# Kernel tuning notes

Hardware: AMD Instinct MI355X
Metric: run time of the kernel (lower is better)

The kernel has to match this reference:

```python
import jax, jax.numpy as jnp
import numpy as np
from jax import lax

BATCH, FS, DIM = 32, 7, 512
E, TOPK, KD = 4, 2, 4            # experts, top-k, scan directions
N_STATE, DT_RANK = 16, 32
CAP_FACTOR, EPS, AUX_W = 1.25, 1e-6, 0.01


def _layernorm(x, g, b, eps=1e-5):
    mu = x.mean(-1, keepdims=True)
    var = ((x - mu) ** 2).mean(-1, keepdims=True)
    return (x - mu) * lax.rsqrt(var + eps) * g + b


def setup_inputs() -> dict:
    key = jax.random.key(0)
    ks = jax.random.split(key, 10)
    s = 0.02
    d = DIM
    return {
        "x": jax.random.normal(ks[0], (BATCH, FS, FS, d), jnp.float32),
        "w_gate": jax.random.normal(ks[1], (d, E)) * s,
        "b_gate": jnp.zeros((E,), jnp.float32),
        "in_proj_w": jax.random.normal(ks[2], (E, d, 2 * d)) * s,
        "in_proj_b": jnp.zeros((E, 2 * d), jnp.float32),
        "conv_w": jax.random.normal(ks[3], (E, d, 3, 3)) * s,
        "conv_b": jnp.zeros((E, d), jnp.float32),
        "x_proj_w": jax.random.normal(ks[4], (E, KD, DT_RANK + 2 * N_STATE, d)) * s,
        "dt_proj_w": jax.random.normal(ks[5], (E, KD, d, DT_RANK)) * s,
        "dt_proj_b": jax.random.normal(ks[6], (E, KD, d)) * 0.1,
        "A_log": jnp.log(jax.random.uniform(ks[7], (E, KD, d, N_STATE), minval=1.0, maxval=16.0)),
        "Ds": jnp.ones((E, KD, d), jnp.float32),
        "out_norm_g": jnp.ones((E, d), jnp.float32),
        "out_norm_b": jnp.zeros((E, d), jnp.float32),
        "norm_g": jnp.ones((E, d), jnp.float32),
        "norm_b": jnp.zeros((E, d), jnp.float32),
    }


def _ss2d_expert(x, in_w, in_b, cw, cb, xpw, dtw, dtb, A_log, Ds, og, ob, ng, nb):
    # x: [B,H,W,d]; one SS2D expert (VMamba-style, use_out_proj=False, out_norm=True)
    B, H, W, d = x.shape
    L = H * W
    xz = x @ in_w + in_b                      # [B,H,W,2d]
    xin, z = jnp.split(xz, 2, axis=-1)
    xc = jnp.transpose(xin, (0, 3, 1, 2))     # [B,d,H,W]
    xc = lax.conv_general_dilated(xc, cw[:, None, :, :], (1, 1), 'SAME',
                                  feature_group_count=d,
                                  dimension_numbers=('NCHW', 'OIHW', 'NCHW'))
    xc = jax.nn.silu(xc + cb[None, :, None, None])
    xh = xc.reshape(B, d, L)                              # row-major (h)
    xv = jnp.transpose(xc, (0, 1, 3, 2)).reshape(B, d, L)  # col-major (v)
    xs = jnp.stack([xh, xh[..., ::-1], xv, xv[..., ::-1]], axis=1)  # [B,K,d,L]

    x_dbl = jnp.einsum('bkdl,kcd->bkcl', xs, xpw)
    dt, Bm, Cm = jnp.split(x_dbl, [DT_RANK, DT_RANK + N_STATE], axis=2)
    dt = jnp.einsum('bkrl,kdr->bkdl', dt, dtw) + dtb[None, :, :, None]
    dt = jax.nn.softplus(dt)                  # [B,K,d,L]
    A = -jnp.exp(A_log)                       # [K,d,N]

    def step(h, inp):
        dt_t, B_t, C_t, x_t = inp             # [B,K,d],[B,K,N],[B,K,N],[B,K,d]
        h = h * jnp.exp(dt_t[..., None] * A) + (dt_t * x_t)[..., None] * B_t[:, :, None, :]
        y = jnp.einsum('bkdn,bkn->bkd', h, C_t)
        return h, y

    h0 = jnp.zeros((B, KD, d, N_STATE), x.dtype)
    seq = (jnp.moveaxis(dt, 3, 0), jnp.moveaxis(Bm, 3, 0),
           jnp.moveaxis(Cm, 3, 0), jnp.moveaxis(xs, 3, 0))
    _, ys = lax.scan(step, h0, seq)           # [L,B,K,d]
    ys = jnp.moveaxis(ys, 0, 3) + Ds[None, :, :, None] * xs  # [B,K,d,L]

    y = ys[:, 0] + ys[:, 1, :, ::-1]
    yv = ys[:, 2] + ys[:, 3, :, ::-1]
    y = y + jnp.transpose(yv.reshape(B, d, W, H), (0, 1, 3, 2)).reshape(B, d, L)
    y = jnp.transpose(y.reshape(B, d, H, W), (0, 2, 3, 1))   # [B,H,W,d]
    y = _layernorm(y, og, ob) * jax.nn.silu(z)
    pooled = y.mean(axis=(1, 2))              # adaptive avg pool -> [B,d]
    return _layernorm(pooled, ng, nb)


def reference(x, w_gate, b_gate, in_proj_w, in_proj_b, conv_w, conv_b, x_proj_w,
              dt_proj_w, dt_proj_b, A_log, Ds, out_norm_g, out_norm_b, norm_g, norm_b):
    B = x.shape[0]
    # gate on globally pooled features
    x_flat = x.mean(axis=(1, 2))                              # [B,dim]
    raw = jax.nn.softmax(x_flat @ w_gate + b_gate, axis=-1)   # [B,E]
    capacity = int(CAP_FACTOR * B)
    _, idx = lax.top_k(raw, TOPK)
    mask = jax.nn.one_hot(idx, E, dtype=raw.dtype).sum(axis=1)  # [B,E]
    masked = raw * mask
    denom = masked.sum(0, keepdims=True) + EPS
    gate_scores = masked / denom * capacity
    importance = raw.mean(0)
    load = mask.mean(0)
    aux_loss = AUX_W * jnp.mean((load - importance) ** 2)

    topv, topi = lax.top_k(gate_scores, TOPK)                 # [B,k]
    # dense dispatch: run every expert on the full batch (E small), then gather
    all_out = jax.vmap(_ss2d_expert, in_axes=(None,) + (0,) * 13)(
        x, in_proj_w, in_proj_b, conv_w, conv_b, x_proj_w, dt_proj_w, dt_proj_b,
        A_log, Ds, out_norm_g, out_norm_b, norm_g, norm_b)    # [E,B,dim]
    sel = all_out[topi, jnp.arange(B)[:, None]]               # [B,k,dim]
    mixed = (topv[..., None] * sel).sum(axis=1)               # [B,dim]
    return mixed, aux_loss
```

## Files before the change

### kernel.cpp

```cpp
#include <hip/hip_runtime.h>
#include <hip/hip_bf16.h>

#define B_   32
#define D_   512
#define L_   49
#define E_   4
#define KD_  4
#define NS_  16
#define RK_  32
#define JOBS_ 64

typedef short s16x8 __attribute__((ext_vector_type(8)));
typedef float f32x4v __attribute__((ext_vector_type(4)));
union U4 { uint4 u; s16x8 s; unsigned short us[8]; };

__device__ __forceinline__ float bf2f(unsigned short u){
  union{unsigned int i; float f;} v; v.i = ((unsigned int)u)<<16; return v.f;
}
__device__ __forceinline__ float2 bfp(unsigned int u){
  union{unsigned int i; float f;} a, b; a.i = u<<16; b.i = u & 0xffff0000u;
  return make_float2(a.f, b.f);
}
__device__ __forceinline__ unsigned short f2bfu(float f){
  union{float f; unsigned int i;} u; u.f = f;
  unsigned int r = u.i + 0x7fffu + ((u.i >> 16) & 1u);
  return (unsigned short)(r >> 16);
}
__device__ __forceinline__ float silu_f(float x){ return x / (1.f + expf(-x)); }

__device__ __forceinline__ float fast_exp2(float x){
  return __builtin_amdgcn_exp2f(x);
}
__device__ __forceinline__ float quad_add4(float y){
  float t1 = __uint_as_float(__builtin_amdgcn_mov_dpp(__float_as_uint(y), 0xB1, 0xF, 0xF, true));
  y += t1;
  float t2 = __uint_as_float(__builtin_amdgcn_mov_dpp(__float_as_uint(y), 0x4E, 0xF, 0xF, true));
  y += t2;
  return y;
}
__device__ __forceinline__ unsigned cvtpk_bf16(float lo, float hi){
  unsigned r; asm("v_cvt_pk_bf16_f32 %0, %1, %2" : "=v"(r) : "v"(lo), "v"(hi)); return r;
}

__device__ __forceinline__ int detect_bf(const void* x){
  unsigned short u = ((const unsigned short*)x)[threadIdx.x & 63];
  int e = (u >> 7) & 0xff;
  unsigned long long m = __ballot(e >= 96 && e < 160);
  return __popcll(m) >= 56;
}

__device__ __forceinline__ float ldf(const void* p, size_t i, int bf){
  return bf ? bf2f(((const unsigned short*)p)[i]) : ((const float*)p)[i];
}
struct f8s{ float v[8]; };
__device__ __forceinline__ f8s ldf8(const void* p, size_t i, int bf){
  f8s r;
  if (bf){
    uint4 u = *(const uint4*)((const unsigned short*)p + i);
    float2 x = bfp(u.x), y = bfp(u.y), z = bfp(u.z), w = bfp(u.w);
    r.v[0]=x.x; r.v[1]=x.y; r.v[2]=y.x; r.v[3]=y.y;
    r.v[4]=z.x; r.v[5]=z.y; r.v[6]=w.x; r.v[7]=w.y;
  } else {
    const float4* q = (const float4*)((const float*)p + i);
    float4 a = q[0], b = q[1];
    r.v[0]=a.x; r.v[1]=a.y; r.v[2]=a.z; r.v[3]=a.w;
    r.v[4]=b.x; r.v[5]=b.y; r.v[6]=b.z; r.v[7]=b.w;
  }
  return r;
}
struct f4s{ float v[4]; };
__device__ __forceinline__ f4s ldf4(const void* p, size_t i, int bf){
  f4s r;
  if (bf){
    uint2 u = *(const uint2*)((const unsigned short*)p + i);
    float2 a = bfp(u.x), b = bfp(u.y);
    r.v[0]=a.x; r.v[1]=a.y; r.v[2]=b.x; r.v[3]=b.y;
  } else {
    float4 a = *(const float4*)((const float*)p + i);
    r.v[0]=a.x; r.v[1]=a.y; r.v[2]=a.z; r.v[3]=a.w;
  }
  return r;
}
__device__ __forceinline__ U4 ldbf8(const void* p, size_t i, int bf){
  U4 r;
  if (bf){
    r.u = *(const uint4*)((const unsigned short*)p + i);
  } else {
    const float* q = (const float*)p + i;
    float4 a = *(const float4*)q, b = *(const float4*)(q+4);
    r.u.x = (unsigned)f2bfu(a.x) | ((unsigned)f2bfu(a.y) << 16);
    r.u.y = (unsigned)f2bfu(a.z) | ((unsigned)f2bfu(a.w) << 16);
    r.u.z = (unsigned)f2bfu(b.x) | ((unsigned)f2bfu(b.y) << 16);
    r.u.w = (unsigned)f2bfu(b.z) | ((unsigned)f2bfu(b.w) << 16);
  }
  return r;
}
__device__ __forceinline__ void split8(const float av[8], U4& hi, U4& lo){
  #pragma unroll
  for (int j = 0; j < 8; j++){
    union{float f; unsigned int i;} u; u.f = av[j];
    unsigned short h = (unsigned short)(u.i >> 16);
    hi.us[j] = h;
    lo.us[j] = f2bfu(av[j] - bf2f(h));
  }
}

__device__ __forceinline__ int dirmap(int k, int l){
  if (k == 0) return l;
  if (k == 1) return 48 - l;
  if (k == 2) return (l % 7) * 7 + l / 7;
  int l2 = 48 - l; return (l2 % 7) * 7 + l2 / 7;
}

__global__ __launch_bounds__(256) void k_prep(const void* __restrict__ x,
                                              const void* __restrict__ w,
                                              const void* __restrict__ wg,
                                              const void* __restrict__ bg,
                                              unsigned short* __restrict__ wt,
                                              unsigned short* __restrict__ xbf,
                                              float* __restrict__ logits){
  __shared__ unsigned short tile[64][72];
  __shared__ float red[4][4];
  __shared__ float pool[4][512];
  int bf = detect_bf(x);
  int blk = blockIdx.x;
  int t = threadIdx.x;
  if (blk < 512){
    int e = blk >> 7, cb = (blk >> 3) & 15, db = blk & 7;
    #pragma unroll
    for (int r = 0; r < 4; r++){
      int d  = r*16 + (t>>4);
      int c0 = (t&15)*4;
      size_t g = ((size_t)e*512 + db*64 + d)*1024 + cb*64 + c0;
      if (bf){
        uint2 u = *(const uint2*)((const unsigned short*)w + g);
        tile[c0+0][d] = (unsigned short)(u.x & 0xffffu);
        tile[c0+1][d] = (unsigned short)(u.x >> 16);
        tile[c0+2][d] = (unsigned short)(u.y & 0xffffu);
        tile[c0+3][d] = (unsigned short)(u.y >> 16);
      } else {
        float4 v = *(const float4*)((const float*)w + g);
        tile[c0+0][d] = f2bfu(v.x);
        tile[c0+1][d] = f2bfu(v.y);
        tile[c0+2][d] = f2bfu(v.z);
        tile[c0+3][d] = f2bfu(v.w);
      }
    }
    __syncthreads();
    #pragma unroll
    for (int r = 0; r < 2; r++){
      int o = r*256 + t;
      int c = o >> 3, d0 = (o & 7)*8;
      uint4 v = *(const uint4*)&tile[c][d0];
      *(uint4*)(wt + ((size_t)e*1024 + cb*64 + c)*512 + db*64 + d0) = v;
    }
  } else {
    int b = blk - 512;
    int wave = t >> 6, lane = t & 63;
    int d0 = lane * 8;
    float s8[8] = {};
    for (int l = wave; l < L_; l += 4){
      size_t ix = ((size_t)(b*L_ + l))*D_ + d0;
      U4 xb;
      if (bf){
        xb.u = *(const uint4*)((const unsigned short*)x + ix);
        float2 a = bfp(xb.u.x), bq = bfp(xb.u.y), c = bfp(xb.u.z), dq = bfp(xb.u.w);
        s8[0] += a.x;  s8[1] += a.y;  s8[2] += bq.x; s8[3] += bq.y;
        s8[4] += c.x;  s8[5] += c.y;  s8[6] += dq.x; s8[7] += dq.y;
      } else {
        const float* q = (const float*)x + ix;
        float4 f0 = *(const float4*)q, f1 = *(const float4*)(q+4);
        float av[8] = {f0.x,f0.y,f0.z,f0.w, f1.x,f1.y,f1.z,f1.w};
        #pragma unroll
        for (int j = 0; j < 8; j++){ xb.us[j] = f2bfu(av[j]); s8[j] += av[j]; }
      }
      *(uint4*)(xbf + ix) = xb.u;
    }
    #pragma unroll
    for (int j = 0; j < 8; j++) pool[wave][d0+j] = s8[j];
    __syncthreads();
    float p[4] = {0.f, 0.f, 0.f, 0.f};
    #pragma unroll
    for (int rep = 0; rep < 2; rep++){
      int d = t + rep*256;
      float s = pool[0][d] + pool[1][d] + pool[2][d] + pool[3][d];
      float xfd = s * (1.f/49.f);
      #pragma unroll
      for (int e = 0; e < 4; e++) p[e] = fmaf(xfd, ldf(wg, (size_t)d*E_ + e, bf), p[e]);
    }
    #pragma unroll
    for (int off = 32; off > 0; off >>= 1){
      #pragma unroll
      for (int e = 0; e < 4; e++) p[e] += __shfl_down(p[e], off, 64);
    }
    if (lane == 0){
      #pragma unroll
      for (int e = 0; e < 4; e++) red[wave][e] = p[e];
    }
    __syncthreads();
    if (t < 4)
      logits[b*4 + t] = red[0][t]+red[1][t]+red[2][t]+red[3][t] + ldf(bg, t, bf);
  }
}

__global__ __launch_bounds__(128) void k_gate2(const void* __restrict__ x,
                                               const float* __restrict__ logits,
                                               int* __restrict__ topi, float* __restrict__ topv,
                                               void* __restrict__ out){
  __shared__ float raw[B_*E_];
  __shared__ int   sel[B_];
  __shared__ float den[E_], auxp[E_];
  int bf = detect_bf(x);
  int t = threadIdx.x;
  if (t < B_){
    float l0=logits[t*4+0], l1=logits[t*4+1], l2=logits[t*4+2], l3=logits[t*4+3];
    float m = fmaxf(fmaxf(l0,l1), fmaxf(l2,l3));
    float e0=expf(l0-m), e1=expf(l1-m), e2=expf(l2-m), e3=expf(l3-m);
    float s = e0+e1+e2+e3;
    float r[4] = {e0/s, e1/s, e2/s, e3/s};
    int i1 = 0; float v1 = r[0];
    for (int e = 1; e < 4; e++) if (r[e] > v1){ v1 = r[e]; i1 = e; }
    int i2 = -1; float v2 = -1.f;
    for (int e = 0; e < 4; e++){ if (e == i1) continue; if (r[e] > v2){ v2 = r[e]; i2 = e; } }
    if (i1 < 0 || i1 > 3) i1 = 0;
    if (i2 < 0 || i2 > 3) i2 = (i1 + 1) & 3;
    sel[t] = (1<<i1) | (1<<i2);
    for (int e = 0; e < 4; e++) raw[t*4+e] = r[e];
  }
  __syncthreads();
  if (t < E_){
    float dn = 0.f, imp = 0.f, ld = 0.f;
    for (int b = 0; b < B_; b++){
      float r = raw[b*4+t];
      int bit = (sel[b] >> t) & 1;
      if (bit) dn += r;
      imp += r; ld += (float)bit;
    }
    den[t] = dn + 1e-6f;
    imp *= (1.f/B_); ld *= (1.f/B_);
    float df = ld - imp; auxp[t] = df*df;
  }
  __syncthreads();
  if (t == 0){
    float a = 0.01f * 0.25f * (auxp[0]+auxp[1]+auxp[2]+auxp[3]);
    if (bf) ((unsigned short*)out)[16384] = f2bfu(a);
    else    ((float*)out)[16384] = a;
  }
  if (t < B_){
    float gs[4];
    for (int e = 0; e < 4; e++){
      int bit = (sel[t] >> e) & 1;
      gs[e] = bit ? raw[t*4+e] * 40.f / den[e] : 0.f;
    }
    int i1 = 0; float v1 = gs[0];
    for (int e = 1; e < 4; e++) if (gs[e] > v1){ v1 = gs[e]; i1 = e; }
    int i2 = -1; float v2 = -1e30f;
    for (int e = 0; e < 4; e++){ if (e == i1) continue; if (gs[e] > v2){ v2 = gs[e]; i2 = e; } }
    if (i1 < 0 || i1 > 3) i1 = 0;
    if (i2 < 0 || i2 > 3) i2 = (i1 + 1) & 3;
    topi[t*2+0] = i1; topv[t*2+0] = v1;
    topi[t*2+1] = i2; topv[t*2+1] = v2;
  }
}

__global__ __launch_bounds__(256, 4) void k_inproj_mfma(const void* __restrict__ x,
                                                     const unsigned short* __restrict__ xbf,
                                                     const unsigned short* __restrict__ wt,
                                                     const void* __restrict__ bias,
                                                     const void* __restrict__ cw,
                                                     const void* __restrict__ cb,
                                                     const int* __restrict__ topi,
                                                     unsigned short* __restrict__ zbuf,
                                                     float* __restrict__ xc,
                                                     unsigned short* __restrict__ xchi,
                                                     unsigned short* __restrict__ xclo){
  __shared__ unsigned short smem[2*4096];
  float* xzt = (float*)smem;
  int bf = detect_bf(x);
  int job = blockIdx.x, nt = blockIdx.y;
  int b = job >> 1;
  int e = topi[job];
  int t = threadIdx.x;
  int wave = t >> 6, lane = t & 63;
  int l16 = lane & 15, quad = lane >> 4;
  int arow = wave*16 + l16; if (arow > 48) arow = 48;
  size_t abase = ((size_t)(b*L_ + arow))*D_;
  int ct = nt*64;
  const unsigned short* wsrc = wt + (size_t)(e*1024 + ct)*512;
  f32x4v acc[4] = {};
  #pragma unroll
  for (int cc = 0; cc < 2; cc++){
    int c = t + cc*256;
    int col = c >> 3, ko8 = c & 7;
    uint4 v = *(const uint4*)(wsrc + (size_t)col*512 + ko8*8);
    *(uint4*)(smem + col*64 + ((ko8 ^ (col & 7))*8)) = v;
  }
  U4 aA, aB;
  aA.u = *(const uint4*)(xbf + abase + quad*8);
  aB.u = *(const uint4*)(xbf + abase + 32 + quad*8);
  __syncthreads();
  for (int s = 0; s < 8; s++){
    unsigned short* cur = smem + (s & 1)*4096;
    U4 nA, nB;
    if (s < 7){
      unsigned short* nxt = smem + ((s+1) & 1)*4096;
      int k0n = (s+1)*64;
      #pragma unroll
      for (int cc = 0; cc < 2; cc++){
        int c = t + cc*256;
        int col = c >> 3, ko8 = c & 7;
        uint4 v = *(const uint4*)(wsrc + (size_t)col*512 + k0n + ko8*8);
        *(uint4*)(nxt + col*64 + ((ko8 ^ (col & 7))*8)) = v;
      }
      nA.u = *(const uint4*)(xbf + abase + k0n + quad*8);
      nB.u = *(const uint4*)(xbf + abase + k0n + 32 + quad*8);
    }
    {
      int ko8 = quad;
      #pragma unroll
      for (int ss = 0; ss < 4; ss++){
        int col = ss*16 + l16;
        U4 bb; bb.u = *(const uint4*)(cur + col*64 + ((ko8 ^ (col & 7))*8));
        acc[ss] = __builtin_amdgcn_mfma_f32_16x16x32_bf16(aA.s, bb.s, acc[ss], 0, 0, 0);
      }
      ko8 = 4 + quad;
      #pragma unroll
      for (int ss = 0; ss < 4; ss++){
        int col = ss*16 + l16;
        U4 bb; bb.u = *(const uint4*)(cur + col*64 + ((ko8 ^ (col & 7))*8));
        acc[ss] = __builtin_amdgcn_mfma_f32_16x16x32_bf16(aB.s, bb.s, acc[ss], 0, 0, 0);
      }
    }
    aA = nA; aB = nB;
    __syncthreads();
  }
  int rb = wave*16 + quad*4;
  if (nt >= 8){
    #pragma unroll
    for (int s = 0; s < 4; s++){
      int c = ct + s*16 + l16;
      float bv = ldf(bias, (size_t)e*1024 + c, bf);
      #pragma unroll
      for (int r = 0; r < 4; r++){
        int row = rb + r;
        if (row < L_)
          zbuf[(size_t)job*25088 + row*D_ + (c - 512)] = f2bfu(acc[s][r] + bv);
      }
    }
    return;
  }
  #pragma unroll
  for (int s = 0; s < 4; s++){
    int cl = s*16 + l16;
    float bv = ldf(bias, (size_t)e*1024 + ct + cl, bf);
    #pragma unroll
    for (int r = 0; r < 4; r++){
      int row = rb + r;
      if (row < L_) xzt[row*68 + cl] = acc[s][r] + bv;
    }
  }
  __syncthreads();
  int c = t & 63, pg = t >> 6;
  int dch = ct + c;
  float wv[9];
  #pragma unroll
  for (int j = 0; j < 9; j++) wv[j] = ldf(cw, ((size_t)(e*D_ + dch))*9 + j, bf);
  float cbv = ldf(cb, (size_t)e*D_ + dch, bf);
  for (int p = pg; p < L_; p += 4){
    int h = p / 7, w = p % 7;
    float a2 = cbv;
    #pragma unroll
    for (int dy = 0; dy < 3; dy++){
      int hh = h + dy - 1; if (hh < 0 || hh >= 7) continue;
      #pragma unroll
      for (int dx = 0; dx < 3; dx++){
        int ww = w + dx - 1; if (ww < 0 || ww >= 7) continue;
        a2 = fmaf(xzt[(hh*7+ww)*68 + c], wv[dy*3+dx], a2);
      }
    }
    float sv = a2 * (1.f/(1.f+expf(-a2)));
    size_t oix = (size_t)job*25088 + (size_t)p*D_ + dch;
    xc[oix] = sv;
    unsigned int ui = __float_as_uint(sv);
    unsigned short hh2 = (unsigned short)(ui >> 16);
    xchi[oix] = hh2;
    xclo[oix] = f2bfu(sv - bf2f(hh2));
  }
}

__global__ __launch_bounds__(256, 4) void k_xproj(const void* __restrict__ x,
                                               const void* __restrict__ xpw,
                                               const int* __restrict__ topi,
                                               const unsigned short* __restrict__ xchi,
                                               const unsigned short* __restrict__ xclo,
                                               float* __restrict__ xdbl){
  __shared__ unsigned short smem[2*4096];
  int bf = detect_bf(x);
  int kq = blockIdx.x, job = blockIdx.y;
  int k = kq & 3, q = kq >> 2;
  int t = threadIdx.x;
  int wave = t >> 6, lane = t & 63;
  int l16 = lane & 15, quad = lane >> 4;
  int e = topi[job];
  int arow = q*16 + l16; if (arow > 48) arow = 48;
  int m = dirmap(k, arow);
  const unsigned short* ahp = xchi + (size_t)job*25088 + (size_t)m*D_;
  const unsigned short* alp = xclo + (size_t)job*25088 + (size_t)m*D_;
  size_t bsrc = ((size_t)(e*KD_+k))*64*512;
  int col16 = wave*16 + l16;
  f32x4v acc = {};
  #pragma unroll
  for (int cc = 0; cc < 2; cc++){
    int c = t + cc*256;
    int col = c >> 3, ko8 = c & 7;
    U4 v = ldbf8(xpw, bsrc + (size_t)col*512 + ko8*8, bf);
    *(uint4*)(smem + col*64 + ((ko8 ^ (col & 7))*8)) = v.u;
  }
  U4 hA, hB, lA, lB;
  hA.u = *(const uint4*)(ahp + quad*8);
  lA.u = *(const uint4*)(alp + quad*8);
  hB.u = *(const uint4*)(ahp + 32 + quad*8);
  lB.u = *(const uint4*)(alp + 32 + quad*8);
  __syncthreads();
  for (int s = 0; s < 8; s++){
    unsigned short* cur = smem + (s & 1)*4096;
    U4 nhA, nhB, nlA, nlB;
    if (s < 7){
      unsigned short* nxt = smem + ((s+1) & 1)*4096;
      int k0n = (s+1)*64;
      #pragma unroll
      for (int cc = 0; cc < 2; cc++){
        int c = t + cc*256;
        int col = c >> 3, ko8 = c & 7;
        U4 v = ldbf8(xpw, bsrc + (size_t)col*512 + k0n + ko8*8, bf);
        *(uint4*)(nxt + col*64 + ((ko8 ^ (col & 7))*8)) = v.u;
      }
      nhA.u = *(const uint4*)(ahp + k0n + quad*8);
      nlA.u = *(const uint4*)(alp + k0n + quad*8);
      nhB.u = *(const uint4*)(ahp + k0n + 32 + quad*8);
      nlB.u = *(const uint4*)(alp + k0n + 32 + quad*8);
    }
    {
      int ko8 = quad;
      U4 bb;  bb.u  = *(const uint4*)(cur + col16*64 + ((ko8 ^ (col16 & 7))*8));
      acc = __builtin_amdgcn_mfma_f32_16x16x32_bf16(hA.s, bb.s, acc, 0, 0, 0);
      acc = __builtin_amdgcn_mfma_f32_16x16x32_bf16(lA.s, bb.s, acc, 0, 0, 0);
      ko8 = 4 + quad;
      U4 bb2; bb2.u = *(const uint4*)(cur + col16*64 + ((ko8 ^ (col16 & 7))*8));
      acc = __builtin_amdgcn_mfma_f32_16x16x32_bf16(hB.s, bb2.s, acc, 0, 0, 0);
      acc = __builtin_amdgcn_mfma_f32_16x16x32_bf16(lB.s, bb2.s, acc, 0, 0, 0);
    }
    hA = nhA; hB = nhB; lA = nlA; lB = nlB;
    __syncthreads();
  }
  float* outb = xdbl + ((size_t)(job*KD_+k))*3136;
  int rb = q*16 + quad*4;
  int c = wave*16 + l16;
  #pragma unroll
  for (int r = 0; r < 4; r++){
    int row = rb + r;
    if (row < L_) outb[row*64 + c] = acc[r];
  }
}

__global__ __launch_bounds__(256, 2) void k_scan(const void* __restrict__ x,
                                              const void* __restrict__ dtw,
                                              const void* __restrict__ dtb_,
                                              const void* __restrict__ alog,
                                              const void* __restrict__ ds_,
                                              const int* __restrict__ topi,
                                              const float* __restrict__ xc,
                                              const float* __restrict__ xdbl,
                                              unsigned short* __restrict__ ybuf){
  int bf = detect_bf(x);
  int kz = blockIdx.x, job = blockIdx.y;
  int k = kz & 3, dz2 = kz >> 2;
  int t = threadIdx.x;
  int e = topi[job];
  int ek = e*KD_ + k;
  __shared__ float bc[49*32];
  __shared__ float dtl[49*260];
  const float* xdb = xdbl + ((size_t)(job*KD_+k))*3136;
  {
    const float4* src4 = (const float4*)xdb;
    for (int i = t; i < 392; i += 256){
      int row = i >> 3, c = i & 7;
      ((float4*)bc)[row*8 + c] = src4[row*16 + 8 + c];
    }
  }
  int w = t >> 6, lane = t & 63;
  {
    int l16 = lane & 15, quad4 = lane >> 4;
    U4 Bv[4];
    #pragma unroll
    for (int nt = 0; nt < 4; nt++){
      int d = dz2*256 + w*64 + nt*16 + l16;
      Bv[nt] = ldbf8(dtw, ((size_t)ek*D_ + d)*RK_ + quad4*8, bf);
    }
    f32x4v acc[4][4] = {};
    #pragma unroll
    for (int rt = 0; rt < 4; rt++){
      int arow = rt*16 + l16; if (arow > 48) arow = 48;
      const float* ap = xdb + arow*64 + quad4*8;
      float4 f0 = *(const float4*)ap, f1 = *(const float4*)(ap+4);
      float av[8] = {f0.x,f0.y,f0.z,f0.w, f1.x,f1.y,f1.z,f1.w};
      U4 Ahi, Alo;
      split8(av, Ahi, Alo);
      #pragma unroll
      for (int nt = 0; nt < 4; nt++){
        acc[rt][nt] = __builtin_amdgcn_mfma_f32_16x16x32_bf16(Ahi.s, Bv[nt].s, acc[rt][nt], 0, 0, 0);
        acc[rt][nt] = __builtin_amdgcn_mfma_f32_16x16x32_bf16(Alo.s, Bv[nt].s, acc[rt][nt], 0, 0, 0);
      }
    }
    #pragma unroll
    for (int nt = 0; nt < 4; nt++){
      int d = dz2*256 + w*64 + nt*16 + l16;
      float bias = ldf(dtb_, (size_t)ek*D_ + d, bf);
      int dloc = w*64 + nt*16 + l16;
      #pragma unroll
      for (int rt = 0; rt < 4; rt++){
        #pragma unroll
        for (int r = 0; r < 4; r++){
          int l = rt*16 + quad4*4 + r;
          if (l < L_){
            float v = acc[rt][nt][r] + bias;
            dtl[l*260 + dloc] = fmaxf(v, 0.f) + __logf(1.f + __expf(-fabsf(v)));
          }
        }
      }
    }
  }
  int q4 = (lane >> 2) * 4;
  int ng = lane & 3;
  int dgl = dz2*256 + w*64 + q4;
  float A2[4][4], Dsv[4];
  #pragma unroll
  for (int jj = 0; jj < 4; jj++){
    int dj = dgl + jj;
    f4s ar = ldf4(alog, ((size_t)ek*D_ + dj)*NS_ + ng*4, bf);
    #pragma unroll
    for (int n = 0; n < 4; n++) A2[jj][n] = -expf(ar.v[n]) * 1.44269504f;
    Dsv[jj] = ldf(ds_, (size_t)ek*D_ + dj, bf);
  }
  __syncthreads();
  float h[4][4];
  #pragma unroll
  for (int jj = 0; jj < 4; jj++)
    #pragma unroll
    for (int n = 0; n < 4; n++) h[jj][n] = 0.f;
  const float* xcb = xc + (size_t)job*25088;
  unsigned short* yb = ybuf + ((size_t)(job*KD_ + k))*25088;
  int dtbase = w*64 + q4;
  for (int c0 = 0; c0 < 49; c0 += 7){
    float4 xv[7];
    #pragma unroll
    for (int j = 0; j < 7; j++){
      int m = dirmap(k, c0 + j);
      xv[j] = *(const float4*)(xcb + (size_t)m*D_ + dgl);
    }
    #pragma unroll
    for (int j = 0; j < 7; j++){
      int l = c0 + j;
      float4 dt4 = *(const float4*)&dtl[l*260 + dtbase];
      float4 B4 = *(const float4*)&bc[l*32 + ng*4];
      float4 C4 = *(const float4*)&bc[l*32 + 16 + ng*4];
      float Ba[4] = {B4.x, B4.y, B4.z, B4.w};
      float Ca[4] = {C4.x, C4.y, C4.z, C4.w};
      float dta[4] = {dt4.x, dt4.y, dt4.z, dt4.w};
      float xa[4]  = {xv[j].x, xv[j].y, xv[j].z, xv[j].w};
      float ys[4];
      #pragma unroll
      for (int jj = 0; jj < 4; jj++){
        float dt = dta[jj], x_t = xa[jj];
        float dtx = dt * x_t;
        float y = 0.f;
        #pragma unroll
        for (int n = 0; n < 4; n++){
          float en = fast_exp2(dt * A2[jj][n]);
          h[jj][n] = fmaf(h[jj][n], en, dtx * Ba[n]);
          y = fmaf(h[jj][n], Ca[n], y);
        }
        y = quad_add4(y);
        ys[jj] = fmaf(Dsv[jj], x_t, y);
      }
      if (ng == 0){
        uint2 o;
        o.x = cvtpk_bf16(ys[0], ys[1]);
        o.y = cvtpk_bf16(ys[2], ys[3]);
        *(uint2*)(yb + (size_t)l*D_ + dgl) = o;
      }
    }
  }
}

__global__ __launch_bounds__(512) void k_final_a(const void* __restrict__ x,
                                                 const void* __restrict__ og,
                                                 const void* __restrict__ ob,
                                                 const int* __restrict__ topi,
                                                 const unsigned short* __restrict__ ybuf,
                                                 const unsigned short* __restrict__ zbuf,
                                                 float* __restrict__ partial){
  __shared__ float pool[8][512];
  int bf = detect_bf(x);
  int job = blockIdx.x, q = blockIdx.y, t = threadIdx.x;
  int wave = t >> 6, lane = t & 63;
  int e = topi[job];
  int d0 = lane*8;
  const unsigned short* yb = ybuf + (size_t)job*KD_*25088;
  const unsigned short* zb = zbuf + (size_t)job*25088;
  float g[8], o[8];
  {
    f8s gg = ldf8(og, (size_t)e*D_ + d0, bf);
    f8s oo = ldf8(ob, (size_t)e*D_ + d0, bf);
    #pragma unroll
    for (int j = 0; j < 8; j++){ g[j] = gg.v[j]; o[j] = oo.v[j]; }
  }
  float acc[8] = {};
  for (int i = wave; i <= 12; i += 8){
    int p = q + 4*i;
    if (p >= L_) break;
    float v[8] = {};
    #pragma unroll
    for (int k = 0; k < KD_; k++){
      int l = dirmap(k, p);
      U4 r; r.u = *(const uint4*)(yb + (size_t)k*25088 + (size_t)l*D_ + d0);
      #pragma unroll
      for (int j = 0; j < 8; j++) v[j] += bf2f(r.us[j]);
    }
    float s = 0.f, ss = 0.f;
    #pragma unroll
    for (int j = 0; j < 8; j++){ s += v[j]; ss += v[j]*v[j]; }
    #pragma unroll
    for (int off = 32; off > 0; off >>= 1){
      s  += __shfl_xor(s,  off, 64);
      ss += __shfl_xor(ss, off, 64);
    }
    float mu = s*(1.f/512.f);
    float var = ss*(1.f/512.f) - mu*mu;
    float rs = rsqrtf(var + 1e-5f);
    U4 zz; zz.u = *(const uint4*)(zb + (size_t)p*D_ + d0);
    #pragma unroll
    for (int j = 0; j < 8; j++){
      float zv = bf2f(zz.us[j]);
      acc[j] += ((v[j]-mu)*rs*g[j] + o[j]) * silu_f(zv);
    }
  }
  #pragma unroll
  for (int j = 0; j < 8; j++) pool[wave][d0+j] = acc[j];
  __syncthreads();
  float pd = pool[0][t]+pool[1][t]+pool[2][t]+pool[3][t]
           + pool[4][t]+pool[5][t]+pool[6][t]+pool[7][t];
  partial[((size_t)(job*4 + q))*512 + t] = pd;
}

__global__ __launch_bounds__(512) void k_finmix(const void* __restrict__ x,
                                                const void* __restrict__ ngg,
                                                const void* __restrict__ nbb,
                                                const int* __restrict__ topi,
                                                const float* __restrict__ topv,
                                                const float* __restrict__ partial,
                                                void* __restrict__ out){
  __shared__ float red[32];
  int bf = detect_bf(x);
  int b = blockIdx.x, t = threadIdx.x;
  int wave = t >> 6, lane = t & 63;
  int j0 = 2*b, j1 = 2*b + 1;
  int e0 = topi[j0], e1 = topi[j1];
  float g0 = topv[j0], g1 = topv[j1];
  const float* p0 = partial + (size_t)j0*4*512;
  const float* p1 = partial + (size_t)j1*4*512;
  float pd0 = (p0[t] + p0[512+t] + p0[1024+t] + p0[1536+t]) * (1.f/49.f);
  float pd1 = (p1[t] + p1[512+t] + p1[1024+t] + p1[1536+t]) * (1.f/49.f);
  float s0 = pd0, ss0 = pd0*pd0, s1 = pd1, ss1 = pd1*pd1;
  #pragma unroll
  for (int off = 32; off > 0; off >>= 1){
    s0  += __shfl_down(s0,  off, 64);
    ss0 += __shfl_down(ss0, off, 64);
    s1  += __shfl_down(s1,  off, 64);
    ss1 += __shfl_down(ss1, off, 64);
  }
  if (lane == 0){
    red[wave] = s0; red[8+wave] = ss0; red[16+wave] = s1; red[24+wave] = ss1;
  }
  __syncthreads();
  s0 = red[0]+red[1]+red[2]+red[3]+red[4]+red[5]+red[6]+red[7];
  ss0 = red[8]+red[9]+red[10]+red[11]+red[12]+red[13]+red[14]+red[15];
  s1 = red[16]+red[17]+red[18]+red[19]+red[20]+red[21]+red[22]+red[23];
  ss1 = red[24]+red[25]+red[26]+red[27]+red[28]+red[29]+red[30]+red[31];
  float mu0 = s0*(1.f/512.f), var0 = ss0*(1.f/512.f) - mu0*mu0;
  float rs0 = rsqrtf(var0 + 1e-5f);
  float mu1 = s1*(1.f/512.f), var1 = ss1*(1.f/512.f) - mu1*mu1;
  float rs1 = rsqrtf(var1 + 1e-5f);
  float v0 = ((pd0-mu0)*rs0*ldf(ngg, (size_t)e0*D_+t, bf) + ldf(nbb, (size_t)e0*D_+t, bf)) * g0;
  float v1 = ((pd1-mu1)*rs1*ldf(ngg, (size_t)e1*D_+t, bf) + ldf(nbb, (size_t)e1*D_+t, bf)) * g1;
  float v = v0 + v1;
  if (bf) ((unsigned short*)out)[b*D_ + t] = f2bfu(v);
  else    ((float*)out)[b*D_ + t] = v;
}

extern "C" void kernel_launch(void* const* d_in, const int* in_sizes, int n_in,
                              void* d_out, int out_size, void* d_ws, size_t ws_size,
                              hipStream_t stream){
  const void* x    = d_in[0];
  const void* wg   = d_in[1];
  const void* bg   = d_in[2];
  const void* ipw  = d_in[3];
  const void* ipb  = d_in[4];
  const void* cw   = d_in[5];
  const void* cb   = d_in[6];
  const void* xpw  = d_in[7];
  const void* dtw  = d_in[8];
  const void* dtb  = d_in[9];
  const void* alog = d_in[10];
  const void* dss  = d_in[11];
  const void* ogg  = d_in[12];
  const void* obb  = d_in[13];
  const void* ngg  = d_in[14];
  const void* nbb  = d_in[15];
  float* wsf = (float*)d_ws;
  int*   topi  = (int*)d_ws + 16;
  float* topv  = wsf + 96;
  float* logits= wsf + 256;
  float* xc    = wsf + 16640;
  float* xdbl  = wsf + 1622272;
  unsigned short* zbuf = (unsigned short*)(wsf + 2425088);
  unsigned short* ybuf   = (unsigned short*)(wsf + 3260672);
  unsigned short* wtrans = ybuf;
  unsigned short* xchi   = ybuf + 2097152;
  unsigned short* xclo   = ybuf + 3702784;
  unsigned short* xbf    = ybuf + 5308416;
  float* partial = wsf + 6471936;

  k_prep  <<<544, 256, 0, stream>>>(x, ipw, wg, bg, wtrans, xbf, logits);
  k_gate2 <<<1, 128, 0, stream>>>(x, logits, topi, topv, d_out);
  k_inproj_mfma<<<dim3(64,16), 256, 0, stream>>>(x, xbf, wtrans, ipb, cw, cb, topi, zbuf, xc, xchi, xclo);
  k_xproj <<<dim3(16,64), 256, 0, stream>>>(x, xpw, topi, xchi, xclo, xdbl);
  k_scan  <<<dim3(8,64), 256, 0, stream>>>(x, dtw, dtb, alog, dss, topi, xc, xdbl, ybuf);
  k_final_a<<<dim3(64,4), 512, 0, stream>>>(x, ogg, obb, topi, ybuf, zbuf, partial);
  k_finmix<<<32, 512, 0, stream>>>(x, ngg, nbb, topi, topv, partial, d_out);
}
```

Before: 191.2 us.

## Fuse x_proj GEMM into scan kernel, keeping x_dbl in shared memory

Removes the separate k_xproj kernel and computes the x_proj projection inside k_scan. The weights are staged through the dtl shared buffer and the result is kept in a shared xdl tile. This drops one kernel launch and the global write and read of xdbl. In exchange, each scan block does the full 49-row projection serially, and the two d-halves per (job,k) duplicate that work.

After: 193.9 us. No clear change (+1.4%).

```diff
diff --git a/kernel.cpp b/kernel.cpp
--- a/kernel.cpp
+++ b/kernel.cpp
@@ -388,89 +388,16 @@
   }
 }
 
-__global__ __launch_bounds__(256, 4) void k_xproj(const void* __restrict__ x,
-                                               const void* __restrict__ xpw,
-                                               const int* __restrict__ topi,
-                                               const unsigned short* __restrict__ xchi,
-                                               const unsigned short* __restrict__ xclo,
-                                               float* __restrict__ xdbl){
-  __shared__ unsigned short smem[2*4096];
-  int bf = detect_bf(x);
-  int kq = blockIdx.x, job = blockIdx.y;
-  int k = kq & 3, q = kq >> 2;
-  int t = threadIdx.x;
-  int wave = t >> 6, lane = t & 63;
-  int l16 = lane & 15, quad = lane >> 4;
-  int e = topi[job];
-  int arow = q*16 + l16; if (arow > 48) arow = 48;
-  int m = dirmap(k, arow);
-  const unsigned short* ahp = xchi + (size_t)job*25088 + (size_t)m*D_;
-  const unsigned short* alp = xclo + (size_t)job*25088 + (size_t)m*D_;
-  size_t bsrc = ((size_t)(e*KD_+k))*64*512;
-  int col16 = wave*16 + l16;
-  f32x4v acc = {};
-  #pragma unroll
-  for (int cc = 0; cc < 2; cc++){
-    int c = t + cc*256;
-    int col = c >> 3, ko8 = c & 7;
-    U4 v = ldbf8(xpw, bsrc + (size_t)col*512 + ko8*8, bf);
-    *(uint4*)(smem + col*64 + ((ko8 ^ (col & 7))*8)) = v.u;
-  }
-  U4 hA, hB, lA, lB;
-  hA.u = *(const uint4*)(ahp + quad*8);
-  lA.u = *(const uint4*)(alp + quad*8);
-  hB.u = *(const uint4*)(ahp + 32 + quad*8);
-  lB.u = *(const uint4*)(alp + 32 + quad*8);
-  __syncthreads();
-  for (int s = 0; s < 8; s++){
-    unsigned short* cur = smem + (s & 1)*4096;
-    U4 nhA, nhB, nlA, nlB;
-    if (s < 7){
-      unsigned short* nxt = smem + ((s+1) & 1)*4096;
-      int k0n = (s+1)*64;
-      #pragma unroll
-      for (int cc = 0; cc < 2; cc++){
-        int c = t + cc*256;
-        int col = c >> 3, ko8 = c & 7;
-        U4 v = ldbf8(xpw, bsrc + (size_t)col*512 + k0n + ko8*8, bf);
-        *(uint4*)(nxt + col*64 + ((ko8 ^ (col & 7))*8)) = v.u;
-      }
-      nhA.u = *(const uint4*)(ahp + k0n + quad*8);
-      nlA.u = *(const uint4*)(alp + k0n + quad*8);
-      nhB.u = *(const uint4*)(ahp + k0n + 32 + quad*8);
-      nlB.u = *(const uint4*)(alp + k0n + 32 + quad*8);
-    }
-    {
-      int ko8 = quad;
-      U4 bb;  bb.u  = *(const uint4*)(cur + col16*64 + ((ko8 ^ (col16 & 7))*8));
-      acc = __builtin_amdgcn_mfma_f32_16x16x32_bf16(hA.s, bb.s, acc, 0, 0, 0);
-      acc = __builtin_amdgcn_mfma_f32_16x16x32_bf16(lA.s, bb.s, acc, 0, 0, 0);
-      ko8 = 4 + quad;
-      U4 bb2; bb2.u = *(const uint4*)(cur + col16*64 + ((ko8 ^ (col16 & 7))*8));
-      acc = __builtin_amdgcn_mfma_f32_16x16x32_bf16(hB.s, bb2.s, acc, 0, 0, 0);
-      acc = __builtin_amdgcn_mfma_f32_16x16x32_bf16(lB.s, bb2.s, acc, 0, 0, 0);
-    }
-    hA = nhA; hB = nhB; lA = nlA; lB = nlB;
-    __syncthreads();
-  }
-  float* outb = xdbl + ((size_t)(job*KD_+k))*3136;
-  int rb = q*16 + quad*4;
-  int c = wave*16 + l16;
-  #pragma unroll
-  for (int r = 0; r < 4; r++){
-    int row = rb + r;
-    if (row < L_) outb[row*64 + c] = acc[r];
-  }
-}
-
 __global__ __launch_bounds__(256, 2) void k_scan(const void* __restrict__ x,
+                                              const void* __restrict__ xpw,
                                               const void* __restrict__ dtw,
                                               const void* __restrict__ dtb_,
                                               const void* __restrict__ alog,
                                               const void* __restrict__ ds_,
                                               const int* __restrict__ topi,
                                               const float* __restrict__ xc,
-                                              const float* __restrict__ xdbl,
+                                              const unsigned short* __restrict__ xchi,
+                                              const unsigned short* __restrict__ xclo,
                                               unsigned short* __restrict__ ybuf){
   int bf = detect_bf(x);
   int kz = blockIdx.x, job = blockIdx.y;
@@ -478,19 +405,75 @@
   int t = threadIdx.x;
   int e = topi[job];
   int ek = e*KD_ + k;
-  __shared__ float bc[49*32];
+  __shared__ float xdl[49*64];
   __shared__ float dtl[49*260];
-  const float* xdb = xdbl + ((size_t)(job*KD_+k))*3136;
+  unsigned short* stg = (unsigned short*)dtl;
+  int w = t >> 6, lane = t & 63;
+  int l16 = lane & 15, quad = lane >> 4;
   {
-    const float4* src4 = (const float4*)xdb;
-    for (int i = t; i < 392; i += 256){
-      int row = i >> 3, c = i & 7;
-      ((float4*)bc)[row*8 + c] = src4[row*16 + 8 + c];
-    }
-  }
-  int w = t >> 6, lane = t & 63;
+    const unsigned short* ahp[4];
+    const unsigned short* alp[4];
+    #pragma unroll
+    for (int q = 0; q < 4; q++){
+      int arow = q*16 + l16; if (arow > 48) arow = 48;
+      int m = dirmap(k, arow);
+      ahp[q] = xchi + (size_t)job*25088 + (size_t)m*D_;
+      alp[q] = xclo + (size_t)job*25088 + (size_t)m*D_;
+    }
+    size_t bsrc = ((size_t)ek)*64*512;
+    int col16 = w*16 + l16;
+    f32x4v acc[4] = {};
+    #pragma unroll
+    for (int cc = 0; cc < 2; cc++){
+      int c = t + cc*256;
+      int col = c >> 3, ko8 = c & 7;
+      U4 v = ldbf8(xpw, bsrc + (size_t)col*512 + ko8*8, bf);
+      *(uint4*)(stg + col*64 + ((ko8 ^ (col & 7))*8)) = v.u;
+    }
+    __syncthreads();
+    for (int s = 0; s < 8; s++){
+      unsigned short* cur = stg + (s & 1)*4096;
+      if (s < 7){
+        unsigned short* nxt = stg + ((s+1) & 1)*4096;
+        int k0n = (s+1)*64;
+        #pragma unroll
+        for (int cc = 0; cc < 2; cc++){
+          int c = t + cc*256;
+          int col = c >> 3, ko8 = c & 7;
+          U4 v = ldbf8(xpw, bsrc + (size_t)col*512 + k0n + ko8*8, bf);
+          *(uint4*)(nxt + col*64 + ((ko8 ^ (col & 7))*8)) = v.u;
+        }
+      }
+      int k0 = s*64;
+      int ko8a = quad, ko8b = 4 + quad;
+      U4 bb;  bb.u  = *(const uint4*)(cur + col16*64 + ((ko8a ^ (col16 & 7))*8));
+      U4 bb2; bb2.u = *(const uint4*)(cur + col16*64 + ((ko8b ^ (col16 & 7))*8));
+      #pragma unroll
+      for (int q = 0; q < 4; q++){
+        U4 hA, lA, hB, lB;
+        hA.u = *(const uint4*)(ahp[q] + k0 + quad*8);
+        lA.u = *(const uint4*)(alp[q] + k0 + quad*8);
+        hB.u = *(const uint4*)(ahp[q] + k0 + 32 + quad*8);
+        lB.u = *(const uint4*)(alp[q] + k0 + 32 + quad*8);
+        acc[q] = __builtin_amdgcn_mfma_f32_16x16x32_bf16(hA.s, bb.s,  acc[q], 0, 0, 0);
+        acc[q] = __builtin_amdgcn_mfma_f32_16x16x32_bf16(lA.s, bb.s,  acc[q], 0, 0, 0);
+        acc[q] = __builtin_amdgcn_mfma_f32_16x16x32_bf16(hB.s, bb2.s, acc[q], 0, 0, 0);
+        acc[q] = __builtin_amdgcn_mfma_f32_16x16x32_bf16(lB.s, bb2.s, acc[q], 0, 0, 0);
+      }
+      __syncthreads();
+    }
+    #pragma unroll
+    for (int q = 0; q < 4; q++){
+      #pragma unroll
+      for (int r = 0; r < 4; r++){
+        int row = q*16 + quad*4 + r;
+        if (row < L_) xdl[row*64 + col16] = acc[q][r];
+      }
+    }
+    __syncthreads();
+  }
   {
-    int l16 = lane & 15, quad4 = lane >> 4;
+    int quad4 = lane >> 4;
     U4 Bv[4];
     #pragma unroll
     for (int nt = 0; nt < 4; nt++){
@@ -501,7 +484,7 @@
     #pragma unroll
     for (int rt = 0; rt < 4; rt++){
       int arow = rt*16 + l16; if (arow > 48) arow = 48;
-      const float* ap = xdb + arow*64 + quad4*8;
+      const float* ap = &xdl[arow*64 + quad4*8];
       float4 f0 = *(const float4*)ap, f1 = *(const float4*)(ap+4);
       float av[8] = {f0.x,f0.y,f0.z,f0.w, f1.x,f1.y,f1.z,f1.w};
       U4 Ahi, Alo;
@@ -512,6 +495,7 @@
         acc[rt][nt] = __builtin_amdgcn_mfma_f32_16x16x32_bf16(Alo.s, Bv[nt].s, acc[rt][nt], 0, 0, 0);
       }
     }
+    __syncthreads();
     #pragma unroll
     for (int nt = 0; nt < 4; nt++){
       int d = dz2*256 + w*64 + nt*16 + l16;
@@ -562,8 +546,8 @@
     for (int j = 0; j < 7; j++){
       int l = c0 + j;
       float4 dt4 = *(const float4*)&dtl[l*260 + dtbase];
-      float4 B4 = *(const float4*)&bc[l*32 + ng*4];
-      float4 C4 = *(const float4*)&bc[l*32 + 16 + ng*4];
+      float4 B4 = *(const float4*)&xdl[l*64 + 32 + ng*4];
+      float4 C4 = *(const float4*)&xdl[l*64 + 48 + ng*4];
       float Ba[4] = {B4.x, B4.y, B4.z, B4.w};
       float Ca[4] = {C4.x, C4.y, C4.z, C4.w};
       float dta[4] = {dt4.x, dt4.y, dt4.z, dt4.w};
@@ -722,7 +706,6 @@
   float* topv  = wsf + 96;
   float* logits= wsf + 256;
   float* xc    = wsf + 16640;
-  float* xdbl  = wsf + 1622272;
   unsigned short* zbuf = (unsigned short*)(wsf + 2425088);
   unsigned short* ybuf   = (unsigned short*)(wsf + 3260672);
   unsigned short* wtrans = ybuf;
@@ -734,8 +717,7 @@
   k_prep  <<<544, 256, 0, stream>>>(x, ipw, wg, bg, wtrans, xbf, logits);
   k_gate2 <<<1, 128, 0, stream>>>(x, logits, topi, topv, d_out);
   k_inproj_mfma<<<dim3(64,16), 256, 0, stream>>>(x, xbf, wtrans, ipb, cw, cb, topi, zbuf, xc, xchi, xclo);
-  k_xproj <<<dim3(16,64), 256, 0, stream>>>(x, xpw, topi, xchi, xclo, xdbl);
-  k_scan  <<<dim3(8,64), 256, 0, stream>>>(x, dtw, dtb, alog, dss, topi, xc, xdbl, ybuf);
+  k_scan  <<<dim3(8,64), 256, 0, stream>>>(x, xpw, dtw, dtb, alog, dss, topi, xc, xchi, xclo, ybuf);
   k_final_a<<<dim3(64,4), 512, 0, stream>>>(x, ogg, obb, topi, ybuf, zbuf, partial);
   k_finmix<<<32, 512, 0, stream>>>(x, ngg, nbb, topi, topv, partial, d_out);
 }
```
